# Optimization experiments

Hardware: AMD Instinct MI355X
Metric: run time of the kernel (lower is better)

## Reference

```python
import jax, jax.numpy as jnp
import numpy as np

B, CH1, CH2, HID, T, E = 64, 3, 4, 16, 16384, 512

def setup_inputs() -> dict:
    key = jax.random.key(0)
    ks = jax.random.split(key, 12)
    s_t = 1.0 / np.sqrt(T)   # fan_in = input_dim for q/k/v projections
    s_e = 1.0 / np.sqrt(E)   # fan_in = embed_dim for out_proj
    return {
        "x":  jax.random.normal(ks[0], (B, 7, T), jnp.float32),
        "W1": jax.random.normal(ks[1], (HID, CH1), jnp.float32) / np.sqrt(CH1),
        "W2": jax.random.normal(ks[2], (HID, CH2), jnp.float32) / np.sqrt(CH2),
        "Wq": jax.random.normal(ks[3], (E, T), jnp.float32) * s_t,
        "bq": jnp.zeros((E,), jnp.float32),
        "Wk": jax.random.normal(ks[4], (E, T), jnp.float32) * s_t,
        "bk": jnp.zeros((E,), jnp.float32),
        "Wv": jax.random.normal(ks[5], (E, T), jnp.float32) * s_t,
        "bv": jnp.zeros((E,), jnp.float32),
        "Wo": jax.random.normal(ks[6], (T, E), jnp.float32) * s_e,
        "bo": jnp.zeros((T,), jnp.float32),
        "W3": jax.random.normal(ks[7], (CH1, HID), jnp.float32) / np.sqrt(HID),
    }

def reference(x, W1, W2, Wq, bq, Wk, bk, Wv, bv, Wo, bo, W3):
    p = x[:, :CH1]            # [B,3,T]  narrow(1,0,ch_1)
    c = x[:, 3:3 + CH2]       # [B,4,T]  narrow(1,3,ch_2)
    q = jnp.einsum('oc,bct->bot', W1, p)   # fc_1: [B,16,T]
    cc = jnp.einsum('oc,bct->bot', W2, c)  # fc_2: [B,16,T]
    # CrossAttention: Linears act on last dim (T -> E)
    Q = jnp.einsum('bct,et->bce', q, Wq) + bq    # [B,16,E]
    K = jnp.einsum('bct,et->bce', cc, Wk) + bk   # [B,16,E]
    V = jnp.einsum('bct,et->bce', cc, Wv) + bv   # [B,16,E]
    scale = 1.0 / np.sqrt(HID)                   # nch = 16 query channels
    attn_w = jax.nn.softmax(jnp.einsum('bce,bcf->bef', Q, K) * scale, axis=-1)  # [B,E,E]
    attn = jnp.einsum('bef,bcf->bce', attn_w, V)  # [B,16,E]
    out = jnp.einsum('bce,te->bct', attn, Wo) + bo  # out_proj: [B,16,T]
    y = jnp.einsum('oc,bct->bot', W3, out)          # fc_3: [B,3,T]
    return p + y
```

## Files before the change

### kernel.cpp

```cpp
#include <hip/hip_runtime.h>

#define BB 64
#define TT 16384
#define EE 512

typedef _Float16 half8 __attribute__((ext_vector_type(8)));
typedef float floatx4 __attribute__((ext_vector_type(4)));

static __device__ __forceinline__ half8 cvt_half8(float4 a, float4 b) {
  half8 h;
  h[0] = (_Float16)a.x; h[1] = (_Float16)a.y; h[2] = (_Float16)a.z; h[3] = (_Float16)a.w;
  h[4] = (_Float16)b.x; h[5] = (_Float16)b.y; h[6] = (_Float16)b.z; h[7] = (_Float16)b.w;
  return h;
}

static __device__ __forceinline__ void gload_lds16(const void* g, void* l) {
  __builtin_amdgcn_global_load_lds(
      (const __attribute__((address_space(1))) void*)g,
      (__attribute__((address_space(3))) void*)l, 16, 0, 0);
}

__global__ __launch_bounds__(256) void zero_ws(float4* __restrict__ p) {
  p[blockIdx.x * 256 + threadIdx.x] = (float4){0.f, 0.f, 0.f, 0.f};
}

__global__ __launch_bounds__(256) void proj_gemm(
    const float* __restrict__ x, const float* __restrict__ Wq,
    const float* __restrict__ Wk, const float* __restrict__ Wv,
    float* __restrict__ Xq, float* __restrict__ Xkv)
{
  __shared__ float Abuf[2][64 * 32];
  __shared__ float Bbuf[2][64 * 32];
  const int t = threadIdx.x;
  const int wave = t >> 6, lane = t & 63;
  const int quad = lane >> 4, l16 = lane & 15;

  const int orig = blockIdx.x;
  const int logical = (orig & 7) * 352 + (orig >> 3);
  const int chunk = logical / 88;
  const int tile  = logical - chunk * 88;
  const int k0 = chunk << 9;

  int mtile, ntile, cpb, chan_base, ldout;
  const float* Wsrc;
  float* outC;
  if (tile < 24) {
    mtile = tile >> 3; ntile = tile & 7;
    cpb = 3; chan_base = 0; ldout = 512;
    Wsrc = Wq + (size_t)(ntile * 64) * TT;
    outC = Xq;
  } else {
    const int t2 = tile - 24;
    mtile = t2 >> 4; ntile = t2 & 15;
    cpb = 4; chan_base = 3; ldout = 1024;
    Wsrc = (ntile < 8) ? (Wk + (size_t)(ntile * 64) * TT)
                       : (Wv + (size_t)((ntile - 8) * 64) * TT);
    outC = Xkv;
  }

  const float* aSrc[2];
  const float* bSrc[2];
#pragma unroll
  for (int r = 0; r < 2; ++r) {
    const int i = (r * 4 + wave) * 64 + lane;
    const int row = i >> 3, u = i & 7;
    const int m = mtile * 64 + row;
    const int bidx = (cpb == 3) ? ((m * 21846) >> 16) : (m >> 2);
    const int j = m - bidx * cpb;
    const int swu = (u ^ (row & 7)) << 2;
    aSrc[r] = x + (size_t)(bidx * 7 + chan_base + j) * TT + k0 + swu;
    bSrc[r] = Wsrc + (size_t)row * TT + k0 + swu;
  }

  floatx4 acc[4];
#pragma unroll
  for (int rt = 0; rt < 4; ++rt) acc[rt] = (floatx4){0.f, 0.f, 0.f, 0.f};

#pragma unroll
  for (int r = 0; r < 2; ++r) {
    gload_lds16(aSrc[r], &Abuf[0][(r * 4 + wave) * 256]);
    gload_lds16(bSrc[r], &Bbuf[0][(r * 4 + wave) * 256]);
  }
  __syncthreads();

  int cur = 0;
  const int brow = wave * 16 + l16;
  const int bsw = brow & 7;
  for (int kt = 0; kt < 16; ++kt) {
    if (kt < 15) {
      const int ko = (kt + 1) * 32;
      const int nxt = cur ^ 1;
#pragma unroll
      for (int r = 0; r < 2; ++r) {
        gload_lds16(aSrc[r] + ko, &Abuf[nxt][(r * 4 + wave) * 256]);
        gload_lds16(bSrc[r] + ko, &Bbuf[nxt][(r * 4 + wave) * 256]);
      }
    }
    float4 b0 = *(const float4*)&Bbuf[cur][brow * 32 + ((((quad << 1) | 0) ^ bsw) << 2)];
    float4 b1 = *(const float4*)&Bbuf[cur][brow * 32 + ((((quad << 1) | 1) ^ bsw) << 2)];
    const half8 hb = cvt_half8(b0, b1);
#pragma unroll
    for (int rt = 0; rt < 4; ++rt) {
      const int arow = rt * 16 + l16;
      const int asw = arow & 7;
      float4 a0 = *(const float4*)&Abuf[cur][arow * 32 + ((((quad << 1) | 0) ^ asw) << 2)];
      float4 a1 = *(const float4*)&Abuf[cur][arow * 32 + ((((quad << 1) | 1) ^ asw) << 2)];
      acc[rt] = __builtin_amdgcn_mfma_f32_16x16x32_f16(cvt_half8(a0, a1), hb, acc[rt], 0, 0, 0);
    }
    if (kt < 15) {
      __syncthreads();
      cur ^= 1;
    }
  }

  const int gc = ntile * 64 + wave * 16 + l16;
#pragma unroll
  for (int rt = 0; rt < 4; ++rt) {
    const int gr = mtile * 64 + rt * 16 + quad * 4;
#pragma unroll
    for (int rg = 0; rg < 4; ++rg)
      atomicAdd(&outC[(size_t)(gr + rg) * ldout + gc], acc[rt][rg]);
  }
}

__global__ __launch_bounds__(256) void attn_mid(
    const float* __restrict__ Xq, const float* __restrict__ Xkv,
    const float* __restrict__ W1, const float* __restrict__ W2,
    const float* __restrict__ W3,
    const float* __restrict__ bq, const float* __restrict__ bk,
    const float* __restrict__ bv, _Float16* __restrict__ U)
{
  __shared__ float Ks[16][512];
  __shared__ float VW[3][512];
  __shared__ float Qs[16][64];
  __shared__ float Xs[4][512];
  __shared__ float W1s[48], W2s[64], W3s[48], W32s[12], w3sum[3];
  const int t = threadIdx.x;
  const int b = blockIdx.y;
  const int e0 = blockIdx.x * 64;

  if (t < 48) W1s[t] = W1[t];
  if (t >= 64 && t < 128) W2s[t - 64] = W2[t - 64];
  if (t >= 128 && t < 176) W3s[t - 128] = W3[t - 128];
  __syncthreads();
  if (t < 12) {
    const int o = t >> 2, jj = t & 3;
    float s = 0.f;
    for (int c = 0; c < 16; ++c) s += W3s[o * 16 + c] * W2s[c * 4 + jj];
    W32s[t] = s;
  }
  if (t >= 16 && t < 19) {
    const int o = t - 16;
    float s = 0.f;
    for (int c = 0; c < 16; ++c) s += W3s[o * 16 + c];
    w3sum[o] = s;
  }
  for (int i = t; i < 2048; i += 256) {
    const int jj = i >> 9, f = i & 511;
    Xs[jj][f] = Xkv[(size_t)(b * 4 + jj) * 1024 + f];
  }
  __syncthreads();
  for (int i = t; i < 8192; i += 256) {
    const int c = i >> 9, f = i & 511;
    float s = bk[f];
#pragma unroll
    for (int jj = 0; jj < 4; ++jj) s += W2s[c * 4 + jj] * Xs[jj][f];
    Ks[c][f] = s;
  }
  __syncthreads();
  for (int i = t; i < 2048; i += 256) {
    const int jj = i >> 9, f = i & 511;
    Xs[jj][f] = Xkv[(size_t)(b * 4 + jj) * 1024 + 512 + f];
  }
  __syncthreads();
  for (int i = t; i < 1536; i += 256) {
    const int o = i >> 9, f = i & 511;
    float s = w3sum[o] * bv[f];
#pragma unroll
    for (int jj = 0; jj < 4; ++jj) s += W32s[o * 4 + jj] * Xs[jj][f];
    VW[o][f] = s;
  }
  for (int i = t; i < 1024; i += 256) {
    const int c = i >> 6, el = i & 63;
    float s = bq[e0 + el];
#pragma unroll
    for (int jj = 0; jj < 3; ++jj)
      s += W1s[c * 3 + jj] * Xq[(size_t)(b * 3 + jj) * 512 + e0 + el];
    Qs[c][el] = s;
  }
  __syncthreads();

  const int wave = t >> 6, lane = t & 63;
  float vwr[3][8];
#pragma unroll
  for (int o = 0; o < 3; ++o) {
    float4 va = *(const float4*)&VW[o][lane * 8];
    float4 vb = *(const float4*)&VW[o][lane * 8 + 4];
    vwr[o][0] = va.x; vwr[o][1] = va.y; vwr[o][2] = va.z; vwr[o][3] = va.w;
    vwr[o][4] = vb.x; vwr[o][5] = vb.y; vwr[o][6] = vb.z; vwr[o][7] = vb.w;
  }

  for (int g = 0; g < 4; ++g) {
    const int el0 = wave * 16 + g * 4;
    float s[4][8];
#pragma unroll
    for (int e = 0; e < 4; ++e)
#pragma unroll
      for (int i = 0; i < 8; ++i) s[e][i] = 0.f;
#pragma unroll
    for (int c = 0; c < 16; ++c) {
      float4 k0 = *(const float4*)&Ks[c][lane * 8];
      float4 k1 = *(const float4*)&Ks[c][lane * 8 + 4];
      float4 qv = *(const float4*)&Qs[c][el0];
      float qa[4] = {qv.x, qv.y, qv.z, qv.w};
#pragma unroll
      for (int e = 0; e < 4; ++e) {
        const float q = qa[e];
        s[e][0] += q * k0.x; s[e][1] += q * k0.y; s[e][2] += q * k0.z; s[e][3] += q * k0.w;
        s[e][4] += q * k1.x; s[e][5] += q * k1.y; s[e][6] += q * k1.z; s[e][7] += q * k1.w;
      }
    }
#pragma unroll
    for (int e = 0; e < 4; ++e) {
      float mx = s[e][0];
#pragma unroll
      for (int i = 1; i < 8; ++i) mx = fmaxf(mx, s[e][i]);
#pragma unroll
      for (int off = 32; off; off >>= 1) mx = fmaxf(mx, __shfl_xor(mx, off));
      float p[8], sum = 0.f;
#pragma unroll
      for (int i = 0; i < 8; ++i) { p[i] = __expf(0.25f * (s[e][i] - mx)); sum += p[i]; }
      float u0 = 0.f, u1 = 0.f, u2 = 0.f;
#pragma unroll
      for (int i = 0; i < 8; ++i) {
        u0 += p[i] * vwr[0][i];
        u1 += p[i] * vwr[1][i];
        u2 += p[i] * vwr[2][i];
      }
#pragma unroll
      for (int off = 32; off; off >>= 1) {
        sum += __shfl_xor(sum, off);
        u0  += __shfl_xor(u0, off);
        u1  += __shfl_xor(u1, off);
        u2  += __shfl_xor(u2, off);
      }
      if (lane == 0) {
        const float inv = 1.0f / sum;
        const size_t base = (size_t)b * 3 * 512 + (e0 + el0 + e);
        U[base]        = (_Float16)(u0 * inv);
        U[base + 512]  = (_Float16)(u1 * inv);
        U[base + 1024] = (_Float16)(u2 * inv);
      }
    }
  }
}

__global__ __launch_bounds__(256) void out_gemm(
    const _Float16* __restrict__ U, const float* __restrict__ Wo,
    const float* __restrict__ x, const float* __restrict__ bo,
    const float* __restrict__ W3, float* __restrict__ outY)
{
  __shared__ _Float16 Au[2][64 * 32];
  __shared__ float    Bw[2][64 * 32];
  const int t = threadIdx.x;
  const int wave = t >> 6, lane = t & 63;
  const int quad = lane >> 4, l16 = lane & 15;
  const int mtile = blockIdx.y, ntile = blockIdx.x;

  float w3s[3];
#pragma unroll
  for (int o = 0; o < 3; ++o) {
    float s = 0.f;
#pragma unroll
    for (int c = 0; c < 16; ++c) s += W3[o * 16 + c];
    w3s[o] = s;
  }

  const int ai = wave * 64 + lane;
  const int arow_s = ai >> 2, au = ai & 3;
  const _Float16* aSrc = U + (size_t)(mtile * 64 + arow_s) * EE
                           + ((au ^ (arow_s & 3)) << 3);
  const float* bSrc[2];
#pragma unroll
  for (int r = 0; r < 2; ++r) {
    const int i = (r * 4 + wave) * 64 + lane;
    const int row = i >> 3, u = i & 7;
    bSrc[r] = Wo + (size_t)(ntile * 64 + row) * EE + ((u ^ (row & 7)) << 2);
  }

  floatx4 acc[4];
#pragma unroll
  for (int rt = 0; rt < 4; ++rt) acc[rt] = (floatx4){0.f, 0.f, 0.f, 0.f};

  gload_lds16(aSrc, &Au[0][wave * 512]);
#pragma unroll
  for (int r = 0; r < 2; ++r)
    gload_lds16(bSrc[r], &Bw[0][(r * 4 + wave) * 256]);
  __syncthreads();

  int cur = 0;
  const int brow = wave * 16 + l16;
  const int bsw = brow & 7;
  for (int kt = 0; kt < 16; ++kt) {
    if (kt < 15) {
      const int nxt = cur ^ 1;
      gload_lds16(aSrc + (kt + 1) * 32, &Au[nxt][wave * 512]);
#pragma unroll
      for (int r = 0; r < 2; ++r)
        gload_lds16(bSrc[r] + (kt + 1) * 32, &Bw[nxt][(r * 4 + wave) * 256]);
    }
    float4 b0 = *(const float4*)&Bw[cur][brow * 32 + ((((quad << 1) | 0) ^ bsw) << 2)];
    float4 b1 = *(const float4*)&Bw[cur][brow * 32 + ((((quad << 1) | 1) ^ bsw) << 2)];
    const half8 hb = cvt_half8(b0, b1);
#pragma unroll
    for (int rt = 0; rt < 4; ++rt) {
      const int arow = rt * 16 + l16;
      const half8 ha = *(const half8*)&Au[cur][arow * 32 + ((quad ^ (arow & 3)) << 3)];
      acc[rt] = __builtin_amdgcn_mfma_f32_16x16x32_f16(ha, hb, acc[rt], 0, 0, 0);
    }
    if (kt < 15) {
      __syncthreads();
      cur ^= 1;
    }
  }

  const int tc = ntile * 64 + wave * 16 + l16;
  const float bot = bo[tc];
#pragma unroll
  for (int rt = 0; rt < 4; ++rt) {
    const int gr = mtile * 64 + rt * 16 + quad * 4;
#pragma unroll
    for (int rg = 0; rg < 4; ++rg) {
      const int rr = gr + rg;
      const int bb = rr / 3, oo = rr - bb * 3;
      const float v = acc[rt][rg]
                    + x[(size_t)(bb * 7 + oo) * TT + tc]
                    + w3s[oo] * bot;
      outY[(size_t)rr * TT + tc] = v;
    }
  }
}

extern "C" void kernel_launch(void* const* d_in, const int* in_sizes, int n_in,
                              void* d_out, int out_size, void* d_ws, size_t ws_size,
                              hipStream_t stream) {
  const float* x  = (const float*)d_in[0];
  const float* W1 = (const float*)d_in[1];
  const float* W2 = (const float*)d_in[2];
  const float* Wq = (const float*)d_in[3];
  const float* bq = (const float*)d_in[4];
  const float* Wk = (const float*)d_in[5];
  const float* bk = (const float*)d_in[6];
  const float* Wv = (const float*)d_in[7];
  const float* bv = (const float*)d_in[8];
  const float* Wo = (const float*)d_in[9];
  const float* bo = (const float*)d_in[10];
  const float* W3 = (const float*)d_in[11];
  float* out = (float*)d_out;

  char* ws = (char*)d_ws;
  float* Xq      = (float*)ws;
  float* Xkv     = (float*)(ws + 393216);
  _Float16* U    = (_Float16*)(ws + 1441792);

  zero_ws<<<dim3(352), 256, 0, stream>>>((float4*)ws);

  proj_gemm<<<dim3(2816), 256, 0, stream>>>(x, Wq, Wk, Wv, Xq, Xkv);
  attn_mid<<<dim3(8, BB), 256, 0, stream>>>(Xq, Xkv, W1, W2, W3, bq, bk, bv, U);
  out_gemm<<<dim3(256, 3), 256, 0, stream>>>(U, Wo, x, bo, W3, out);
}
```

Before: 275.2 us.

## Triple-buffer LDS pipelines with vmcnt waits and 2x2 wave tiling

Both GEMM kernels move from double-buffered LDS staging with a full __syncthreads each k-step to a three-stage ring. Loads run two tiles ahead, and fine-grained s_waitcnt vmcnt plus a raw s_barrier let more global loads stay in flight. MFMA sections are wrapped in s_setprio so waves issuing matrix ops get priority. The projection GEMM also changes its wave layout from 4x1 to 2x2, so each wave converts 2 A and 2 B fragments instead of 1 B and 4 A. This cuts LDS reads and fp32-to-half conversions, at the cost of more LDS and the correctness risk of hand-counted vmcnt values.

```diff
diff --git a/kernel.cpp b/kernel.cpp
--- a/kernel.cpp
+++ b/kernel.cpp
@@ -29,11 +29,12 @@
     const float* __restrict__ Wk, const float* __restrict__ Wv,
     float* __restrict__ Xq, float* __restrict__ Xkv)
 {
-  __shared__ float Abuf[2][64 * 32];
-  __shared__ float Bbuf[2][64 * 32];
+  __shared__ float Abuf[3][64 * 32];
+  __shared__ float Bbuf[3][64 * 32];
   const int t = threadIdx.x;
   const int wave = t >> 6, lane = t & 63;
   const int quad = lane >> 4, l16 = lane & 15;
+  const int wr = wave >> 1, wc = wave & 1;
 
   const int orig = blockIdx.x;
   const int logical = (orig & 7) * 352 + (orig >> 3);
@@ -72,54 +73,81 @@
     bSrc[r] = Wsrc + (size_t)row * TT + k0 + swu;
   }
 
-  floatx4 acc[4];
-#pragma unroll
-  for (int rt = 0; rt < 4; ++rt) acc[rt] = (floatx4){0.f, 0.f, 0.f, 0.f};
-
-#pragma unroll
-  for (int r = 0; r < 2; ++r) {
-    gload_lds16(aSrc[r], &Abuf[0][(r * 4 + wave) * 256]);
-    gload_lds16(bSrc[r], &Bbuf[0][(r * 4 + wave) * 256]);
-  }
-  __syncthreads();
+  floatx4 acc[2][2];
+#pragma unroll
+  for (int rt = 0; rt < 2; ++rt)
+#pragma unroll
+    for (int ct = 0; ct < 2; ++ct)
+      acc[rt][ct] = (floatx4){0.f, 0.f, 0.f, 0.f};
+
+  const int sw = l16 & 7;
+
+  auto stage = [&](int kt_, int buf_) {
+    const int ko = kt_ * 32;
+#pragma unroll
+    for (int r = 0; r < 2; ++r) {
+      gload_lds16(aSrc[r] + ko, &Abuf[buf_][(r * 4 + wave) * 256]);
+      gload_lds16(bSrc[r] + ko, &Bbuf[buf_][(r * 4 + wave) * 256]);
+    }
+  };
+  auto compute = [&](int buf_) {
+    half8 hb[2], ha[2];
+#pragma unroll
+    for (int ct = 0; ct < 2; ++ct) {
+      const int brow = wc * 32 + ct * 16 + l16;
+      float4 b0 = *(const float4*)&Bbuf[buf_][brow * 32 + ((((quad << 1) | 0) ^ sw) << 2)];
+      float4 b1 = *(const float4*)&Bbuf[buf_][brow * 32 + ((((quad << 1) | 1) ^ sw) << 2)];
+      hb[ct] = cvt_half8(b0, b1);
+    }
+#pragma unroll
+    for (int rt = 0; rt < 2; ++rt) {
+      const int arow = wr * 32 + rt * 16 + l16;
+      float4 a0 = *(const float4*)&Abuf[buf_][arow * 32 + ((((quad << 1) | 0) ^ sw) << 2)];
+      float4 a1 = *(const float4*)&Abuf[buf_][arow * 32 + ((((quad << 1) | 1) ^ sw) << 2)];
+      ha[rt] = cvt_half8(a0, a1);
+    }
+    __builtin_amdgcn_s_setprio(1);
+#pragma unroll
+    for (int rt = 0; rt < 2; ++rt)
+#pragma unroll
+      for (int ct = 0; ct < 2; ++ct)
+        acc[rt][ct] = __builtin_amdgcn_mfma_f32_16x16x32_f16(ha[rt], hb[ct], acc[rt][ct], 0, 0, 0);
+    __builtin_amdgcn_s_setprio(0);
+  };
+
+  stage(0, 0);
+  stage(1, 1);
+  asm volatile("s_waitcnt vmcnt(4)" ::: "memory");
+  __builtin_amdgcn_s_barrier();
+  __builtin_amdgcn_sched_barrier(0);
 
   int cur = 0;
-  const int brow = wave * 16 + l16;
-  const int bsw = brow & 7;
-  for (int kt = 0; kt < 16; ++kt) {
-    if (kt < 15) {
-      const int ko = (kt + 1) * 32;
-      const int nxt = cur ^ 1;
-#pragma unroll
-      for (int r = 0; r < 2; ++r) {
-        gload_lds16(aSrc[r] + ko, &Abuf[nxt][(r * 4 + wave) * 256]);
-        gload_lds16(bSrc[r] + ko, &Bbuf[nxt][(r * 4 + wave) * 256]);
-      }
-    }
-    float4 b0 = *(const float4*)&Bbuf[cur][brow * 32 + ((((quad << 1) | 0) ^ bsw) << 2)];
-    float4 b1 = *(const float4*)&Bbuf[cur][brow * 32 + ((((quad << 1) | 1) ^ bsw) << 2)];
-    const half8 hb = cvt_half8(b0, b1);
-#pragma unroll
-    for (int rt = 0; rt < 4; ++rt) {
-      const int arow = rt * 16 + l16;
-      const int asw = arow & 7;
-      float4 a0 = *(const float4*)&Abuf[cur][arow * 32 + ((((quad << 1) | 0) ^ asw) << 2)];
-      float4 a1 = *(const float4*)&Abuf[cur][arow * 32 + ((((quad << 1) | 1) ^ asw) << 2)];
-      acc[rt] = __builtin_amdgcn_mfma_f32_16x16x32_f16(cvt_half8(a0, a1), hb, acc[rt], 0, 0, 0);
-    }
-    if (kt < 15) {
-      __syncthreads();
-      cur ^= 1;
-    }
-  }
-
-  const int gc = ntile * 64 + wave * 16 + l16;
-#pragma unroll
-  for (int rt = 0; rt < 4; ++rt) {
-    const int gr = mtile * 64 + rt * 16 + quad * 4;
-#pragma unroll
-    for (int rg = 0; rg < 4; ++rg)
-      atomicAdd(&outC[(size_t)(gr + rg) * ldout + gc], acc[rt][rg]);
+#pragma unroll
+  for (int kt = 0; kt < 14; ++kt) {
+    const int nx2 = (cur + 2 >= 3) ? cur - 1 : cur + 2;
+    stage(kt + 2, nx2);
+    compute(cur);
+    asm volatile("s_waitcnt vmcnt(4)" ::: "memory");
+    __builtin_amdgcn_s_barrier();
+    __builtin_amdgcn_sched_barrier(0);
+    cur = (cur + 1 >= 3) ? 0 : cur + 1;
+  }
+  compute(cur);
+  asm volatile("s_waitcnt vmcnt(0)" ::: "memory");
+  __builtin_amdgcn_s_barrier();
+  __builtin_amdgcn_sched_barrier(0);
+  compute((cur + 1 >= 3) ? 0 : cur + 1);
+
+#pragma unroll
+  for (int rt = 0; rt < 2; ++rt) {
+#pragma unroll
+    for (int ct = 0; ct < 2; ++ct) {
+      const int gr = mtile * 64 + wr * 32 + rt * 16 + quad * 4;
+      const int gc = ntile * 64 + wc * 32 + ct * 16 + l16;
+#pragma unroll
+      for (int rg = 0; rg < 4; ++rg)
+        atomicAdd(&outC[(size_t)(gr + rg) * ldout + gc], acc[rt][ct][rg]);
+    }
   }
 }
 
@@ -260,8 +288,8 @@
     const float* __restrict__ x, const float* __restrict__ bo,
     const float* __restrict__ W3, float* __restrict__ outY)
 {
-  __shared__ _Float16 Au[2][64 * 32];
-  __shared__ float    Bw[2][64 * 32];
+  __shared__ _Float16 Au[3][64 * 32];
+  __shared__ float    Bw[3][64 * 32];
   const int t = threadIdx.x;
   const int wave = t >> 6, lane = t & 63;
   const int quad = lane >> 4, l16 = lane & 15;
@@ -292,37 +320,54 @@
 #pragma unroll
   for (int rt = 0; rt < 4; ++rt) acc[rt] = (floatx4){0.f, 0.f, 0.f, 0.f};
 
-  gload_lds16(aSrc, &Au[0][wave * 512]);
-#pragma unroll
-  for (int r = 0; r < 2; ++r)
-    gload_lds16(bSrc[r], &Bw[0][(r * 4 + wave) * 256]);
-  __syncthreads();
-
-  int cur = 0;
   const int brow = wave * 16 + l16;
   const int bsw = brow & 7;
-  for (int kt = 0; kt < 16; ++kt) {
-    if (kt < 15) {
-      const int nxt = cur ^ 1;
-      gload_lds16(aSrc + (kt + 1) * 32, &Au[nxt][wave * 512]);
-#pragma unroll
-      for (int r = 0; r < 2; ++r)
-        gload_lds16(bSrc[r] + (kt + 1) * 32, &Bw[nxt][(r * 4 + wave) * 256]);
-    }
-    float4 b0 = *(const float4*)&Bw[cur][brow * 32 + ((((quad << 1) | 0) ^ bsw) << 2)];
-    float4 b1 = *(const float4*)&Bw[cur][brow * 32 + ((((quad << 1) | 1) ^ bsw) << 2)];
+
+  auto stage = [&](int kt_, int buf_) {
+    gload_lds16(aSrc + kt_ * 32, &Au[buf_][wave * 512]);
+#pragma unroll
+    for (int r = 0; r < 2; ++r)
+      gload_lds16(bSrc[r] + kt_ * 32, &Bw[buf_][(r * 4 + wave) * 256]);
+  };
+  auto compute = [&](int buf_) {
+    float4 b0 = *(const float4*)&Bw[buf_][brow * 32 + ((((quad << 1) | 0) ^ bsw) << 2)];
+    float4 b1 = *(const float4*)&Bw[buf_][brow * 32 + ((((quad << 1) | 1) ^ bsw) << 2)];
     const half8 hb = cvt_half8(b0, b1);
+    half8 ha[4];
 #pragma unroll
     for (int rt = 0; rt < 4; ++rt) {
       const int arow = rt * 16 + l16;
-      const half8 ha = *(const half8*)&Au[cur][arow * 32 + ((quad ^ (arow & 3)) << 3)];
-      acc[rt] = __builtin_amdgcn_mfma_f32_16x16x32_f16(ha, hb, acc[rt], 0, 0, 0);
-    }
-    if (kt < 15) {
-      __syncthreads();
-      cur ^= 1;
-    }
-  }
+      ha[rt] = *(const half8*)&Au[buf_][arow * 32 + ((quad ^ (arow & 3)) << 3)];
+    }
+    __builtin_amdgcn_s_setprio(1);
+#pragma unroll
+    for (int rt = 0; rt < 4; ++rt)
+      acc[rt] = __builtin_amdgcn_mfma_f32_16x16x32_f16(ha[rt], hb, acc[rt], 0, 0, 0);
+    __builtin_amdgcn_s_setprio(0);
+  };
+
+  stage(0, 0);
+  stage(1, 1);
+  asm volatile("s_waitcnt vmcnt(3)" ::: "memory");
+  __builtin_amdgcn_s_barrier();
+  __builtin_amdgcn_sched_barrier(0);
+
+  int cur = 0;
+#pragma unroll
+  for (int kt = 0; kt < 14; ++kt) {
+    const int nx2 = (cur + 2 >= 3) ? cur - 1 : cur + 2;
+    stage(kt + 2, nx2);
+    compute(cur);
+    asm volatile("s_waitcnt vmcnt(3)" ::: "memory");
+    __builtin_amdgcn_s_barrier();
+    __builtin_amdgcn_sched_barrier(0);
+    cur = (cur + 1 >= 3) ? 0 : cur + 1;
+  }
+  compute(cur);
+  asm volatile("s_waitcnt vmcnt(0)" ::: "memory");
+  __builtin_amdgcn_s_barrier();
+  __builtin_amdgcn_sched_barrier(0);
+  compute((cur + 1 >= 3) ? 0 : cur + 1);
 
   const int tc = ntile * 64 + wave * 16 + l16;
   const float bot = bo[tc];
```

New measurement: 277.0 us. No clear change (+0.6%).
